# Kernel optimization log

Measured on AMD Instinct MI355X. Metric: run time of the kernel, lower is better.

The kernel has to match this reference:

```python
import jax, jax.numpy as jnp
import numpy as np

H = 128
K = 20
N = 100000
B = 65536
TIME_SCALE = 1.0
NEG = -1e9


def setup_inputs() -> dict:
    key = jax.random.key(0)
    ks = jax.random.split(key, 16)
    s = 0.05
    return {
        "edge_index": jax.random.randint(ks[0], (2, B), 0, N),
        "edge_timestamp": jax.random.randint(ks[1], (B,), 0, 1000000),
        "hist_neighbors": jax.random.randint(ks[2], (N, K), 0, N),
        "hist_times": jax.random.randint(ks[3], (N, K), 0, 1000000),
        "hist_signs": jax.random.randint(ks[4], (N, K), 0, 2),
        "node_emb": jax.random.normal(ks[5], (N, H), jnp.float32) * s,
        "sign_emb": jax.random.normal(ks[6], (2, H), jnp.float32) * s,
        "tp_w1": jax.random.normal(ks[7], (H,), jnp.float32) * s,   # Linear(1,H) weight (flattened)
        "tp_b1": jax.random.normal(ks[8], (H,), jnp.float32) * s,
        "tp_w2": jax.random.normal(ks[9], (H, H), jnp.float32) * s,  # stored [in,out]
        "tp_b2": jax.random.normal(ks[10], (H,), jnp.float32) * s,
        "em_w1": jax.random.normal(ks[11], (4 * H, H), jnp.float32) * s,
        "em_b1": jax.random.normal(ks[12], (H,), jnp.float32) * s,
        "em_w2": jax.random.normal(ks[13], (H, 1), jnp.float32) * s,
        "em_b2": jax.random.normal(ks[14], (1,), jnp.float32) * s,
    }


def _encode(node_ids, query_times, hist_neighbors, hist_times, hist_signs,
            node_emb, sign_emb, tp_w1, tp_b1, tp_w2, tp_b2):
    # node_ids, query_times: [B]
    neigh = hist_neighbors[node_ids]   # [B,K]
    times = hist_times[node_ids]       # [B,K]
    signs = hist_signs[node_ids]       # [B,K]
    valid = (neigh != -1) & (times < query_times[:, None])
    neigh_c = jnp.where(neigh == -1, 0, neigh)
    neigh_e = node_emb[neigh_c]        # [B,K,H]
    sign_e = sign_emb[signs]           # [B,K,H]
    delta = (query_times[:, None].astype(jnp.float32) - times.astype(jnp.float32)) / TIME_SCALE
    h = jax.nn.relu(delta[..., None] * tp_w1 + tp_b1)           # [B,K,H]
    time_e = jnp.einsum('bkh,hd->bkd', h, tp_w2) + tp_b2        # [B,K,H]
    keys = neigh_e + sign_e + time_e
    query = node_emb[node_ids][:, None]                          # [B,1,H]
    scores = jnp.sum(query * keys, axis=-1) / jnp.sqrt(jnp.float32(H))
    scores = jnp.where(valid, scores, NEG)
    attn = jax.nn.softmax(scores, axis=1)                        # [B,K]
    return jnp.einsum('bk,bkh->bh', attn, keys)                  # [B,H]


def reference(edge_index, edge_timestamp, hist_neighbors, hist_times, hist_signs,
              node_emb, sign_emb, tp_w1, tp_b1, tp_w2, tp_b2,
              em_w1, em_b1, em_w2, em_b2):
    u, v = edge_index[0], edge_index[1]
    zu = _encode(u, edge_timestamp, hist_neighbors, hist_times, hist_signs,
                 node_emb, sign_emb, tp_w1, tp_b1, tp_w2, tp_b2)
    zv = _encode(v, edge_timestamp, hist_neighbors, hist_times, hist_signs,
                 node_emb, sign_emb, tp_w1, tp_b1, tp_w2, tp_b2)
    feat = jnp.concatenate([zu, zv, jnp.abs(zu - zv), zu * zv], axis=1)  # [B,4H]
    hid = jax.nn.relu(feat @ em_w1 + em_b1)
    logits = (hid @ em_w2 + em_b2).squeeze(-1)                           # [B]
    return logits
```

## Files before the change

### kernel.cpp

```cpp
#include <hip/hip_runtime.h>
#include <hip/hip_bf16.h>
#include <math.h>

#define H 128
#define K 20
#define EPB 16

#define WS_TBL    0
#define WS_THM    65792
#define WS_CNT    66176
#define WSB_HI    67072
#define WSB_LO    99840

typedef __attribute__((ext_vector_type(8))) short short8;
typedef __attribute__((ext_vector_type(4))) float f32x4;

template<int CTRL, int RMASK>
__device__ __forceinline__ float dpp_add(float x) {
  int y = __builtin_amdgcn_update_dpp(0, __float_as_int(x), CTRL, RMASK, 0xf, true);
  return x + __int_as_float(y);
}
__device__ __forceinline__ float wave_sum63(float x) {
  x = dpp_add<0xB1,  0xf>(x);
  x = dpp_add<0x4E,  0xf>(x);
  x = dpp_add<0x141, 0xf>(x);
  x = dpp_add<0x140, 0xf>(x);
  x = dpp_add<0x142, 0xa>(x);
  x = dpp_add<0x143, 0xc>(x);
  return x;
}
__device__ __forceinline__ float bcast63(float x) {
  return __int_as_float(__builtin_amdgcn_readlane(__float_as_int(x), 63));
}

__device__ __forceinline__ unsigned short bfbits(float x) {
  __hip_bfloat16 h = __float2bfloat16(x);
  unsigned short u; __builtin_memcpy(&u, &h, 2); return u;
}
__device__ __forceinline__ float bf2f(unsigned short u) {
  return __uint_as_float(((unsigned)u) << 16);
}

__global__ __launch_bounds__(128) void aux_kernel(
    const float* __restrict__ w1v, const float* __restrict__ b1v,
    const float* __restrict__ w2, const float* __restrict__ b2,
    const float* __restrict__ em_w1, float* __restrict__ ws)
{
  int blk = blockIdx.x;
  int tid = threadIdx.x;
  if (blk < 257) {
    __shared__ float th[H];
    __shared__ int grp[H];
    __shared__ int sidx[2 * H];
    __shared__ int Msh;
    float w = w1v[tid], b = b1v[tid];
    int g = (w > 0.f) ? 0 : ((w < 0.f) ? 1 : 2);
    float t = (g == 2) ? 0.f : (-b / w);
    th[tid] = t; grp[tid] = g;
    if (tid == 0) Msh = 0;
    __syncthreads();
    if (g != 2) {
      int r = 0;
      for (int i = 0; i < H; i++)
        if (grp[i] != 2 && (th[i] < t || (th[i] == t && i < tid))) r++;
      sidx[r] = (tid << 1) | (g == 0 ? 1 : 0);
      atomicAdd(&Msh, 1);
      if (blk == 0) ws[WS_THM + r] = t;
    }
    __syncthreads();
    int M = Msh;
    if (blk == 0 && tid == 0) ((int*)(ws + WS_CNT))[0] = M;
    int r = blk;
    if (r > M) return;
    int d = tid;
    float accW = 0.f, accB = b2[d];
    for (int i = 0; i < H; i++)
      if (grp[i] == 2 && b1v[i] > 0.f) accB += b1v[i] * w2[i * H + d];
    #pragma unroll 4
    for (int i = 0; i < M; i++) {
      int ent = sidx[i];
      int h = ent >> 1;
      int isP = ent & 1;
      int take = (i < r) ? isP : (1 - isP);
      if (take) {
        float wv = w2[h * H + d];
        accW += w1v[h] * wv;
        accB += b1v[h] * wv;
      }
    }
    ws[WS_TBL + r * 256 + 2 * d + 0] = accW;
    ws[WS_TBL + r * 256 + 2 * d + 1] = accB;
  } else {
    int idx = (blk - 257) * 128 + tid;
    int j  = idx & 7;
    int l  = (idx >> 3) & 63;
    int kc = (idx >> 9) & 15;
    int c  = idx >> 13;
    int k = kc * 32 + ((l >> 4) * 8) + j;
    int n = c * 16 + (l & 15);
    float x = em_w1[k * H + n];
    unsigned short hb = bfbits(x);
    unsigned short lb = bfbits(x - bf2f(hb));
    ((unsigned short*)(ws + WSB_HI))[idx] = hb;
    ((unsigned short*)(ws + WSB_LO))[idx] = lb;
  }
}

template<int NB>
__device__ __forceinline__ void run_sides(
    int sbase, int b0, int B, int lane,
    const int* __restrict__ edge_index, const int* __restrict__ edge_ts,
    const int* __restrict__ hist_nb, const int* __restrict__ hist_tm,
    const int* __restrict__ hist_sg,
    const float* __restrict__ node_emb, const float* __restrict__ ws,
    float th0, float th1, float th2, float th3,
    float2 se0, float2 se1, float* __restrict__ zbuf)
{
  const float S = 0.088388347648318447f;
  int eBase = sbase >> 1;
  int eN = b0 + eBase;
  int nU = edge_index[eN];
  int nV = edge_index[B + eN];
  int t_n = edge_ts[eN];
  float2 qU_n = *(const float2*)(node_emb + (size_t)nU * H + 2 * lane);
  float2 qV_n = *(const float2*)(node_emb + (size_t)nV * H + 2 * lane);
  int pkU_n = 0, tmU_n = 0, pkV_n = 0, tmV_n = 0;
  if (lane < K) {
    pkU_n = (hist_nb[nU * K + lane] << 1) | hist_sg[nU * K + lane];
    tmU_n = hist_tm[nU * K + lane];
    pkV_n = (hist_nb[nV * K + lane] << 1) | hist_sg[nV * K + lane];
    tmV_n = hist_tm[nV * K + lane];
  }

  #pragma unroll 1
  for (int p = 0; p < 4; p++) {
    int e = eBase + p;
    int tC = t_n;
    float2 qU = qU_n, qV = qV_n;
    int pkU = pkU_n, tmU = tmU_n, pkV = pkV_n, tmV = tmV_n;
    if (p < 3) {
      int e2 = b0 + e + 1;
      int nU2 = edge_index[e2];
      int nV2 = edge_index[B + e2];
      t_n = edge_ts[e2];
      qU_n = *(const float2*)(node_emb + (size_t)nU2 * H + 2 * lane);
      qV_n = *(const float2*)(node_emb + (size_t)nV2 * H + 2 * lane);
      if (lane < K) {
        pkU_n = (hist_nb[nU2 * K + lane] << 1) | hist_sg[nU2 * K + lane];
        tmU_n = hist_tm[nU2 * K + lane];
        pkV_n = (hist_nb[nV2 * K + lane] << 1) | hist_sg[nV2 * K + lane];
        tmV_n = hist_tm[nV2 * K + lane];
      }
    }

    unsigned long long mU0 = __ballot((lane < K) && (tmU < tC) && (pkU >= 0));
    unsigned long long mV0 = __ballot((lane < K) && (tmV < tC) && (pkV >= 0));
    float qUx = qU.x * S, qUy = qU.y * S;
    float qVx = qV.x * S, qVy = qV.y * S;

    float mxU = -3.0e38f, ssU = 0.f, zU0 = 0.f, zU1 = 0.f;
    float mxV = -3.0e38f, ssV = 0.f, zV0 = 0.f, zV1 = 0.f;
    unsigned long long mU = mU0, mV = mV0;
    while (mU | mV) {
      int kU = mU ? (__ffsll((long long)mU) - 1) : 0;
      int kV = mV ? (__ffsll((long long)mV) - 1) : 0;
      bool vU = mU != 0, vV = mV != 0;
      mU &= mU - 1; mV &= mV - 1;
      int tmkU = __builtin_amdgcn_readlane(tmU, kU);
      int pkkU = __builtin_amdgcn_readlane(pkU, kU);
      int tmkV = __builtin_amdgcn_readlane(tmV, kV);
      int pkkV = __builtin_amdgcn_readlane(pkV, kV);
      float dkU = (float)tC - (float)tmkU;
      float dkV = (float)tC - (float)tmkV;
      int rU = __popcll(__ballot(th0 < dkU)) + __popcll(__ballot(th1 < dkU));
      int rV = __popcll(__ballot(th0 < dkV)) + __popcll(__ballot(th1 < dkV));
      if (NB == 4) {
        rU += __popcll(__ballot(th2 < dkU)) + __popcll(__ballot(th3 < dkU));
        rV += __popcll(__ballot(th2 < dkV)) + __popcll(__ballot(th3 < dkV));
      }
      const float4 tbU = *(const float4*)(ws + WS_TBL + rU * 256 + 4 * lane);
      const float4 tbV = *(const float4*)(ws + WS_TBL + rV * 256 + 4 * lane);
      int nbU = (pkkU < 0) ? 0 : (pkkU >> 1);
      int nbV = (pkkV < 0) ? 0 : (pkkV >> 1);
      float2 neU = *(const float2*)(node_emb + (size_t)nbU * H + 2 * lane);
      float2 neV = *(const float2*)(node_emb + (size_t)nbV * H + 2 * lane);
      float kU0 = neU.x + ((pkkU & 1) ? se1.x : se0.x) + dkU * tbU.x + tbU.y;
      float kU1 = neU.y + ((pkkU & 1) ? se1.y : se0.y) + dkU * tbU.z + tbU.w;
      float kV0 = neV.x + ((pkkV & 1) ? se1.x : se0.x) + dkV * tbV.x + tbV.y;
      float kV1 = neV.y + ((pkkV & 1) ? se1.y : se0.y) + dkV * tbV.z + tbV.w;
      float pU = wave_sum63(qUx * kU0 + qUy * kU1);
      float pV = wave_sum63(qVx * kV0 + qVy * kV1);
      float sU = vU ? bcast63(pU) : -1e9f;
      float sV = vV ? bcast63(pV) : -1e9f;
      float mnU = fmaxf(mxU, sU);
      float alU = __expf(mxU - mnU), peU = __expf(sU - mnU);
      ssU = ssU * alU + peU;
      zU0 = zU0 * alU + peU * kU0;
      zU1 = zU1 * alU + peU * kU1;
      mxU = mnU;
      float mnV = fmaxf(mxV, sV);
      float alV = __expf(mxV - mnV), peV = __expf(sV - mnV);
      ssV = ssV * alV + peV;
      zV0 = zV0 * alV + peV * kV0;
      zV1 = zV1 * alV + peV * kV1;
      mxV = mnV;
    }

    if (mU0) {
      float inv = 1.f / ssU; zU0 *= inv; zU1 *= inv;
    } else {
      zU0 = 0.f; zU1 = 0.f;
      #pragma unroll 1
      for (int k = 0; k < K; k++) {
        int tm_k = __builtin_amdgcn_readlane(tmU, k);
        int pk_k = __builtin_amdgcn_readlane(pkU, k);
        float dk = (float)tC - (float)tm_k;
        int r = __popcll(__ballot(th0 < dk)) + __popcll(__ballot(th1 < dk));
        if (NB == 4)
          r += __popcll(__ballot(th2 < dk)) + __popcll(__ballot(th3 < dk));
        const float4 tb = *(const float4*)(ws + WS_TBL + r * 256 + 4 * lane);
        int nbc = (pk_k < 0) ? 0 : (pk_k >> 1);
        float2 ne = *(const float2*)(node_emb + (size_t)nbc * H + 2 * lane);
        zU0 += ne.x + ((pk_k & 1) ? se1.x : se0.x) + dk * tb.x + tb.y;
        zU1 += ne.y + ((pk_k & 1) ? se1.y : se0.y) + dk * tb.z + tb.w;
      }
      zU0 *= 0.05f; zU1 *= 0.05f;
    }
    if (mV0) {
      float inv = 1.f / ssV; zV0 *= inv; zV1 *= inv;
    } else {
      zV0 = 0.f; zV1 = 0.f;
      #pragma unroll 1
      for (int k = 0; k < K; k++) {
        int tm_k = __builtin_amdgcn_readlane(tmV, k);
        int pk_k = __builtin_amdgcn_readlane(pkV, k);
        float dk = (float)tC - (float)tm_k;
        int r = __popcll(__ballot(th0 < dk)) + __popcll(__ballot(th1 < dk));
        if (NB == 4)
          r += __popcll(__ballot(th2 < dk)) + __popcll(__ballot(th3 < dk));
        const float4 tb = *(const float4*)(ws + WS_TBL + r * 256 + 4 * lane);
        int nbc = (pk_k < 0) ? 0 : (pk_k >> 1);
        float2 ne = *(const float2*)(node_emb + (size_t)nbc * H + 2 * lane);
        zV0 += ne.x + ((pk_k & 1) ? se1.x : se0.x) + dk * tb.x + tb.y;
        zV1 += ne.y + ((pk_k & 1) ? se1.y : se0.y) + dk * tb.z + tb.w;
      }
      zV0 *= 0.05f; zV1 *= 0.05f;
    }

    int sw = (e & 7) << 1;
    int ccU = lane ^ sw;
    int ccV = (64 + lane) ^ sw;
    *(float2*)&zbuf[(e << 8) + (ccU << 1)] = make_float2(zU0, zU1);
    *(float2*)&zbuf[(e << 8) + (ccV << 1)] = make_float2(zV0, zV1);
  }
}

__global__ __launch_bounds__(256, 4) void tgat_main_kernel(
    const int* __restrict__ edge_index, const int* __restrict__ edge_ts,
    const int* __restrict__ hist_nb, const int* __restrict__ hist_tm,
    const int* __restrict__ hist_sg,
    const float* __restrict__ node_emb, const float* __restrict__ sign_emb,
    const float* __restrict__ em_b1,
    const float* __restrict__ em_w2, const float* __restrict__ em_b2,
    const float* __restrict__ ws, float* __restrict__ out, int B)
{
  __shared__ __align__(16) float zbuf[EPB * 256];

  int tid = threadIdx.x;
  int lane = tid & 63;
  int wv = __builtin_amdgcn_readfirstlane(tid >> 6);
  int b0 = blockIdx.x * EPB;

  int M = ((const int*)(ws + WS_CNT))[0];
  float th0 = (lane       < M) ? ws[WS_THM + lane      ] : 3.0e38f;
  float th1 = (lane + 64  < M) ? ws[WS_THM + lane + 64 ] : 3.0e38f;
  float2 se0 = *(const float2*)(sign_emb + 2 * lane);
  float2 se1 = *(const float2*)(sign_emb + H + 2 * lane);

  int sbase = wv * 8;
  if (M <= 128) {
    run_sides<2>(sbase, b0, B, lane, edge_index, edge_ts, hist_nb, hist_tm,
                 hist_sg, node_emb, ws, th0, th1, 3.0e38f, 3.0e38f,
                 se0, se1, zbuf);
  } else {
    float th2 = (lane + 128 < M) ? ws[WS_THM + lane + 128] : 3.0e38f;
    float th3 = (lane + 192 < M) ? ws[WS_THM + lane + 192] : 3.0e38f;
    run_sides<4>(sbase, b0, B, lane, edge_index, edge_ts, hist_nb, hist_tm,
                 hist_sg, node_emb, ws, th0, th1, th2, th3,
                 se0, se1, zbuf);
  }
  __syncthreads();

  const unsigned short* whi = (const unsigned short*)(ws + WSB_HI);
  const unsigned short* wlo = (const unsigned short*)(ws + WSB_LO);
  int c0 = 2 * wv;
  int m_ = lane & 15;
  int qd = lane >> 4;
  int sw = (m_ & 7) << 1;
  const float* zrow = zbuf + (m_ << 8);
  f32x4 acc0 = {0.f, 0.f, 0.f, 0.f};
  f32x4 acc1 = {0.f, 0.f, 0.f, 0.f};
  #pragma unroll
  for (int kc = 0; kc < 16; kc++) {
    const int reg = kc >> 2;
    int cb = (kc & 3) * 16 + qd * 4;
    float av[8];
    if (reg == 0) {
      float4 A0 = *(const float4*)(zrow + (((cb    ) ^ sw) << 1));
      float4 A1 = *(const float4*)(zrow + (((cb + 2) ^ sw) << 1));
      av[0]=A0.x; av[1]=A0.y; av[2]=A0.z; av[3]=A0.w;
      av[4]=A1.x; av[5]=A1.y; av[6]=A1.z; av[7]=A1.w;
    } else if (reg == 1) {
      float4 A0 = *(const float4*)(zrow + (((cb + 64) ^ sw) << 1));
      float4 A1 = *(const float4*)(zrow + (((cb + 66) ^ sw) << 1));
      av[0]=A0.x; av[1]=A0.y; av[2]=A0.z; av[3]=A0.w;
      av[4]=A1.x; av[5]=A1.y; av[6]=A1.z; av[7]=A1.w;
    } else {
      float4 U0 = *(const float4*)(zrow + (((cb    ) ^ sw) << 1));
      float4 U1 = *(const float4*)(zrow + (((cb + 2) ^ sw) << 1));
      float4 V0 = *(const float4*)(zrow + (((cb + 64) ^ sw) << 1));
      float4 V1 = *(const float4*)(zrow + (((cb + 66) ^ sw) << 1));
      float uu[8] = {U0.x,U0.y,U0.z,U0.w,U1.x,U1.y,U1.z,U1.w};
      float vvv[8] = {V0.x,V0.y,V0.z,V0.w,V1.x,V1.y,V1.z,V1.w};
      if (reg == 2) {
        #pragma unroll
        for (int j = 0; j < 8; j++) av[j] = fabsf(uu[j] - vvv[j]);
      } else {
        #pragma unroll
        for (int j = 0; j < 8; j++) av[j] = uu[j] * vvv[j];
      }
    }
    union { short8 v; unsigned short u[8]; } ahi, alo;
    #pragma unroll
    for (int j = 0; j < 8; j++) {
      unsigned short hb = bfbits(av[j]);
      ahi.u[j] = hb;
      alo.u[j] = bfbits(av[j] - bf2f(hb));
    }
    int f0 = (((c0    ) * 16 + kc) * 64 + lane) * 8;
    int f1 = (((c0 + 1) * 16 + kc) * 64 + lane) * 8;
    short8 bh0 = *(const short8*)(whi + f0);
    short8 bl0 = *(const short8*)(wlo + f0);
    short8 bh1 = *(const short8*)(whi + f1);
    short8 bl1 = *(const short8*)(wlo + f1);
    acc0 = __builtin_amdgcn_mfma_f32_16x16x32_bf16(ahi.v, bh0, acc0, 0, 0, 0);
    acc0 = __builtin_amdgcn_mfma_f32_16x16x32_bf16(ahi.v, bl0, acc0, 0, 0, 0);
    acc0 = __builtin_amdgcn_mfma_f32_16x16x32_bf16(alo.v, bh0, acc0, 0, 0, 0);
    acc1 = __builtin_amdgcn_mfma_f32_16x16x32_bf16(ahi.v, bh1, acc1, 0, 0, 0);
    acc1 = __builtin_amdgcn_mfma_f32_16x16x32_bf16(ahi.v, bl1, acc1, 0, 0, 0);
    acc1 = __builtin_amdgcn_mfma_f32_16x16x32_bf16(alo.v, bh1, acc1, 0, 0, 0);
  }
  __syncthreads();

  float* hp = zbuf;
  float eb0 = em_b1[c0 * 16 + m_];
  float eb1 = em_b1[(c0 + 1) * 16 + m_];
  #pragma unroll
  for (int r = 0; r < 4; r++) {
    int edge = qd * 4 + r;
    hp[edge * 132 + c0 * 16 + m_]       = fmaxf(acc0[r] + eb0, 0.f);
    hp[edge * 132 + (c0 + 1) * 16 + m_] = fmaxf(acc1[r] + eb1, 0.f);
  }
  __syncthreads();

  float2 w2v = *(const float2*)(em_w2 + 2 * lane);
  float bias2 = em_b2[0];
  #pragma unroll
  for (int i = 0; i < 4; i++) {
    int e = wv * 4 + i;
    int b = b0 + e;
    float2 hv = *(const float2*)(hp + e * 132 + 2 * lane);
    float p = wave_sum63(hv.x * w2v.x + hv.y * w2v.y);
    float ps = bcast63(p);
    if (lane == 0 && b < B) out[b] = ps + bias2;
  }
}

extern "C" void kernel_launch(void* const* d_in, const int* in_sizes, int n_in,
                              void* d_out, int out_size, void* d_ws, size_t ws_size,
                              hipStream_t stream)
{
  (void)n_in; (void)out_size; (void)ws_size;
  const int* edge_index = (const int*)d_in[0];
  const int* edge_ts    = (const int*)d_in[1];
  const int* hist_nb    = (const int*)d_in[2];
  const int* hist_tm    = (const int*)d_in[3];
  const int* hist_sg    = (const int*)d_in[4];
  const float* node_emb = (const float*)d_in[5];
  const float* sign_emb = (const float*)d_in[6];
  const float* tp_w1    = (const float*)d_in[7];
  const float* tp_b1    = (const float*)d_in[8];
  const float* tp_w2    = (const float*)d_in[9];
  const float* tp_b2    = (const float*)d_in[10];
  const float* em_w1    = (const float*)d_in[11];
  const float* em_b1    = (const float*)d_in[12];
  const float* em_w2    = (const float*)d_in[13];
  const float* em_b2    = (const float*)d_in[14];
  float* out = (float*)d_out;
  float* ws  = (float*)d_ws;
  int B = in_sizes[1];

  hipLaunchKernelGGL(aux_kernel, dim3(769), dim3(128), 0, stream,
                     tp_w1, tp_b1, tp_w2, tp_b2, em_w1, ws);
  int grid = (B + EPB - 1) / EPB;
  hipLaunchKernelGGL(tgat_main_kernel, dim3(grid), dim3(256), 0, stream,
                     edge_index, edge_ts, hist_nb, hist_tm, hist_sg,
                     node_emb, sign_emb, em_b1, em_w2, em_b2, ws, out, B);
}
```

Baseline: 391.9 us.

## Process two neighbors per online-softmax step and merge fallback path into main loop

```diff
diff --git a/kernel.cpp b/kernel.cpp
--- a/kernel.cpp
+++ b/kernel.cpp
@@ -155,97 +155,98 @@
 
     unsigned long long mU0 = __ballot((lane < K) && (tmU < tC) && (pkU >= 0));
     unsigned long long mV0 = __ballot((lane < K) && (tmV < tC) && (pkV >= 0));
+    bool fU = (mU0 == 0), fV = (mV0 == 0);
+    unsigned long long mU = fU ? 0xFFFFFull : mU0;
+    unsigned long long mV = fV ? 0xFFFFFull : mV0;
     float qUx = qU.x * S, qUy = qU.y * S;
     float qVx = qV.x * S, qVy = qV.y * S;
 
     float mxU = -3.0e38f, ssU = 0.f, zU0 = 0.f, zU1 = 0.f;
     float mxV = -3.0e38f, ssV = 0.f, zV0 = 0.f, zV1 = 0.f;
-    unsigned long long mU = mU0, mV = mV0;
     while (mU | mV) {
-      int kU = mU ? (__ffsll((long long)mU) - 1) : 0;
-      int kV = mV ? (__ffsll((long long)mV) - 1) : 0;
-      bool vU = mU != 0, vV = mV != 0;
-      mU &= mU - 1; mV &= mV - 1;
-      int tmkU = __builtin_amdgcn_readlane(tmU, kU);
-      int pkkU = __builtin_amdgcn_readlane(pkU, kU);
-      int tmkV = __builtin_amdgcn_readlane(tmV, kV);
-      int pkkV = __builtin_amdgcn_readlane(pkV, kV);
-      float dkU = (float)tC - (float)tmkU;
-      float dkV = (float)tC - (float)tmkV;
-      int rU = __popcll(__ballot(th0 < dkU)) + __popcll(__ballot(th1 < dkU));
-      int rV = __popcll(__ballot(th0 < dkV)) + __popcll(__ballot(th1 < dkV));
+      bool vUa = mU != 0; int kUa = vUa ? (__ffsll((long long)mU) - 1) : 0; mU &= mU - 1;
+      bool vUb = mU != 0; int kUb = vUb ? (__ffsll((long long)mU) - 1) : 0; mU &= mU - 1;
+      bool vVa = mV != 0; int kVa = vVa ? (__ffsll((long long)mV) - 1) : 0; mV &= mV - 1;
+      bool vVb = mV != 0; int kVb = vVb ? (__ffsll((long long)mV) - 1) : 0; mV &= mV - 1;
+
+      int tmkUa = __builtin_amdgcn_readlane(tmU, kUa);
+      int pkkUa = __builtin_amdgcn_readlane(pkU, kUa);
+      int tmkUb = __builtin_amdgcn_readlane(tmU, kUb);
+      int pkkUb = __builtin_amdgcn_readlane(pkU, kUb);
+      int tmkVa = __builtin_amdgcn_readlane(tmV, kVa);
+      int pkkVa = __builtin_amdgcn_readlane(pkV, kVa);
+      int tmkVb = __builtin_amdgcn_readlane(tmV, kVb);
+      int pkkVb = __builtin_amdgcn_readlane(pkV, kVb);
+
+      float dUa = (float)tC - (float)tmkUa;
+      float dUb = (float)tC - (float)tmkUb;
+      float dVa = (float)tC - (float)tmkVa;
+      float dVb = (float)tC - (float)tmkVb;
+
+      int rUa = __popcll(__ballot(th0 < dUa)) + __popcll(__ballot(th1 < dUa));
+      int rUb = __popcll(__ballot(th0 < dUb)) + __popcll(__ballot(th1 < dUb));
+      int rVa = __popcll(__ballot(th0 < dVa)) + __popcll(__ballot(th1 < dVa));
+      int rVb = __popcll(__ballot(th0 < dVb)) + __popcll(__ballot(th1 < dVb));
       if (NB == 4) {
-        rU += __popcll(__ballot(th2 < dkU)) + __popcll(__ballot(th3 < dkU));
-        rV += __popcll(__ballot(th2 < dkV)) + __popcll(__ballot(th3 < dkV));
+        rUa += __popcll(__ballot(th2 < dUa)) + __popcll(__ballot(th3 < dUa));
+        rUb += __popcll(__ballot(th2 < dUb)) + __popcll(__ballot(th3 < dUb));
+        rVa += __popcll(__ballot(th2 < dVa)) + __popcll(__ballot(th3 < dVa));
+        rVb += __popcll(__ballot(th2 < dVb)) + __popcll(__ballot(th3 < dVb));
       }
-      const float4 tbU = *(const float4*)(ws + WS_TBL + rU * 256 + 4 * lane);
-      const float4 tbV = *(const float4*)(ws + WS_TBL + rV * 256 + 4 * lane);
-      int nbU = (pkkU < 0) ? 0 : (pkkU >> 1);
-      int nbV = (pkkV < 0) ? 0 : (pkkV >> 1);
-      float2 neU = *(const float2*)(node_emb + (size_t)nbU * H + 2 * lane);
-      float2 neV = *(const float2*)(node_emb + (size_t)nbV * H + 2 * lane);
-      float kU0 = neU.x + ((pkkU & 1) ? se1.x : se0.x) + dkU * tbU.x + tbU.y;
-      float kU1 = neU.y + ((pkkU & 1) ? se1.y : se0.y) + dkU * tbU.z + tbU.w;
-      float kV0 = neV.x + ((pkkV & 1) ? se1.x : se0.x) + dkV * tbV.x + tbV.y;
-      float kV1 = neV.y + ((pkkV & 1) ? se1.y : se0.y) + dkV * tbV.z + tbV.w;
-      float pU = wave_sum63(qUx * kU0 + qUy * kU1);
-      float pV = wave_sum63(qVx * kV0 + qVy * kV1);
-      float sU = vU ? bcast63(pU) : -1e9f;
-      float sV = vV ? bcast63(pV) : -1e9f;
-      float mnU = fmaxf(mxU, sU);
-      float alU = __expf(mxU - mnU), peU = __expf(sU - mnU);
-      ssU = ssU * alU + peU;
-      zU0 = zU0 * alU + peU * kU0;
-      zU1 = zU1 * alU + peU * kU1;
+
+      const float4 tUa = *(const float4*)(ws + WS_TBL + rUa * 256 + 4 * lane);
+      const float4 tUb = *(const float4*)(ws + WS_TBL + rUb * 256 + 4 * lane);
+      const float4 tVa = *(const float4*)(ws + WS_TBL + rVa * 256 + 4 * lane);
+      const float4 tVb = *(const float4*)(ws + WS_TBL + rVb * 256 + 4 * lane);
+      int nUa = (pkkUa < 0) ? 0 : (pkkUa >> 1);
+      int nUb = (pkkUb < 0) ? 0 : (pkkUb >> 1);
+      int nVa = (pkkVa < 0) ? 0 : (pkkVa >> 1);
+      int nVb = (pkkVb < 0) ? 0 : (pkkVb >> 1);
+      float2 eUa = *(const float2*)(node_emb + (size_t)nUa * H + 2 * lane);
+      float2 eUb = *(const float2*)(node_emb + (size_t)nUb * H + 2 * lane);
+      float2 eVa = *(const float2*)(node_emb + (size_t)nVa * H + 2 * lane);
+      float2 eVb = *(const float2*)(node_emb + (size_t)nVb * H + 2 * lane);
+
+      float kUa0 = eUa.x + ((pkkUa & 1) ? se1.x : se0.x) + dUa * tUa.x + tUa.y;
+      float kUa1 = eUa.y + ((pkkUa & 1) ? se1.y : se0.y) + dUa * tUa.z + tUa.w;
+      float kUb0 = eUb.x + ((pkkUb & 1) ? se1.x : se0.x) + dUb * tUb.x + tUb.y;
+      float kUb1 = eUb.y + ((pkkUb & 1) ? se1.y : se0.y) + dUb * tUb.z + tUb.w;
+      float kVa0 = eVa.x + ((pkkVa & 1) ? se1.x : se0.x) + dVa * tVa.x + tVa.y;
+      float kVa1 = eVa.y + ((pkkVa & 1) ? se1.y : se0.y) + dVa * tVa.z + tVa.w;
+      float kVb0 = eVb.x + ((pkkVb & 1) ? se1.x : se0.x) + dVb * tVb.x + tVb.y;
+      float kVb1 = eVb.y + ((pkkVb & 1) ? se1.y : se0.y) + dVb * tVb.z + tVb.w;
+
+      float pUa = wave_sum63(qUx * kUa0 + qUy * kUa1);
+      float pUb = wave_sum63(qUx * kUb0 + qUy * kUb1);
+      float pVa = wave_sum63(qVx * kVa0 + qVy * kVa1);
+      float pVb = wave_sum63(qVx * kVb0 + qVy * kVb1);
+
+      float sUa = (vUa && !fU) ? bcast63(pUa) : -1e9f;
+      float sUb = (vUb && !fU) ? bcast63(pUb) : -1e9f;
+      float sVa = (vVa && !fV) ? bcast63(pVa) : -1e9f;
+      float sVb = (vVb && !fV) ? bcast63(pVb) : -1e9f;
+
+      float mnU = fmaxf(mxU, fmaxf(sUa, sUb));
+      float alU = __expf(mxU - mnU);
+      float paU = __expf(sUa - mnU);
+      float pbU = __expf(sUb - mnU);
+      ssU = ssU * alU + paU + pbU;
+      zU0 = zU0 * alU + paU * kUa0 + pbU * kUb0;
+      zU1 = zU1 * alU + paU * kUa1 + pbU * kUb1;
       mxU = mnU;
-      float mnV = fmaxf(mxV, sV);
-      float alV = __expf(mxV - mnV), peV = __expf(sV - mnV);
-      ssV = ssV * alV + peV;
-      zV0 = zV0 * alV + peV * kV0;
-      zV1 = zV1 * alV + peV * kV1;
+
+      float mnV = fmaxf(mxV, fmaxf(sVa, sVb));
+      float alV = __expf(mxV - mnV);
+      float paV = __expf(sVa - mnV);
+      float pbV = __expf(sVb - mnV);
+      ssV = ssV * alV + paV + pbV;
+      zV0 = zV0 * alV + paV * kVa0 + pbV * kVb0;
+      zV1 = zV1 * alV + paV * kVa1 + pbV * kVb1;
       mxV = mnV;
     }
 
-    if (mU0) {
-      float inv = 1.f / ssU; zU0 *= inv; zU1 *= inv;
-    } else {
-      zU0 = 0.f; zU1 = 0.f;
-      #pragma unroll 1
-      for (int k = 0; k < K; k++) {
-        int tm_k = __builtin_amdgcn_readlane(tmU, k);
-        int pk_k = __builtin_amdgcn_readlane(pkU, k);
-        float dk = (float)tC - (float)tm_k;
-        int r = __popcll(__ballot(th0 < dk)) + __popcll(__ballot(th1 < dk));
-        if (NB == 4)
-          r += __popcll(__ballot(th2 < dk)) + __popcll(__ballot(th3 < dk));
-        const float4 tb = *(const float4*)(ws + WS_TBL + r * 256 + 4 * lane);
-        int nbc = (pk_k < 0) ? 0 : (pk_k >> 1);
-        float2 ne = *(const float2*)(node_emb + (size_t)nbc * H + 2 * lane);
-        zU0 += ne.x + ((pk_k & 1) ? se1.x : se0.x) + dk * tb.x + tb.y;
-        zU1 += ne.y + ((pk_k & 1) ? se1.y : se0.y) + dk * tb.z + tb.w;
-      }
-      zU0 *= 0.05f; zU1 *= 0.05f;
-    }
-    if (mV0) {
-      float inv = 1.f / ssV; zV0 *= inv; zV1 *= inv;
-    } else {
-      zV0 = 0.f; zV1 = 0.f;
-      #pragma unroll 1
-      for (int k = 0; k < K; k++) {
-        int tm_k = __builtin_amdgcn_readlane(tmV, k);
-        int pk_k = __builtin_amdgcn_readlane(pkV, k);
-        float dk = (float)tC - (float)tm_k;
-        int r = __popcll(__ballot(th0 < dk)) + __popcll(__ballot(th1 < dk));
-        if (NB == 4)
-          r += __popcll(__ballot(th2 < dk)) + __popcll(__ballot(th3 < dk));
-        const float4 tb = *(const float4*)(ws + WS_TBL + r * 256 + 4 * lane);
-        int nbc = (pk_k < 0) ? 0 : (pk_k >> 1);
-        float2 ne = *(const float2*)(node_emb + (size_t)nbc * H + 2 * lane);
-        zV0 += ne.x + ((pk_k & 1) ? se1.x : se0.x) + dk * tb.x + tb.y;
-        zV1 += ne.y + ((pk_k & 1) ? se1.y : se0.y) + dk * tb.z + tb.w;
-      }
-      zV0 *= 0.05f; zV1 *= 0.05f;
-    }
+    float invU = 1.f / ssU; zU0 *= invU; zU1 *= invU;
+    float invV = 1.f / ssV; zV0 *= invV; zV1 *= invV;
 
     int sw = (e & 7) << 1;
     int ccU = lane ^ sw;
@@ -330,12 +331,16 @@
         for (int j = 0; j < 8; j++) av[j] = uu[j] * vvv[j];
       }
     }
-    union { short8 v; unsigned short u[8]; } ahi, alo;
+    union { short8 v; unsigned u[4]; } ahi, alo;
     #pragma unroll
-    for (int j = 0; j < 8; j++) {
-      unsigned short hb = bfbits(av[j]);
-      ahi.u[j] = hb;
-      alo.u[j] = bfbits(av[j] - bf2f(hb));
+    for (int j = 0; j < 4; j++) {
+      unsigned b0u = __float_as_uint(av[2 * j]);
+      unsigned b1u = __float_as_uint(av[2 * j + 1]);
+      ahi.u[j] = __builtin_amdgcn_perm(b1u, b0u, 0x07060302u);
+      float l0 = av[2 * j]     - __uint_as_float(b0u & 0xFFFF0000u);
+      float l1 = av[2 * j + 1] - __uint_as_float(b1u & 0xFFFF0000u);
+      __hip_bfloat162 lp = __float22bfloat162_rn(make_float2(l0, l1));
+      __builtin_memcpy(&alo.u[j], &lp, 4);
     }
     int f0 = (((c0    ) * 16 + kc) * 64 + lane) * 8;
     int f1 = (((c0 + 1) * 16 + kc) * 64 + lane) * 8;
```

After: 367.9 us. 6.1% less time.
